# Optimization experiments

Hardware: AMD Instinct MI355X
Metric: run time of the kernel (lower is better)

## Reference

```python
import jax, jax.numpy as jnp
import numpy as np

L = 8       # num_layers
D = 512     # embed_dim
H = 8       # num_heads
HD = D // H # head_dim = 64
V = 256     # vocab_size
T = 2048    # seq len (= context_length)
B = 4       # batch
FF = 4 * D  # mlp hidden
EPS = 1e-5


def setup_inputs() -> dict:
    key = jax.random.key(0)
    ks = jax.random.split(key, 18)
    g = lambda k, shape: (jax.random.normal(k, shape, jnp.float32) * 0.02)
    return {
        "x": jax.random.randint(ks[0], (B, T), 0, V),
        "tok_emb": g(ks[1], (V, D)),
        "pos_emb": g(ks[2], (T, D)),
        "attn_w": g(ks[3], (L, D, 3 * D)),
        "attn_b": g(ks[4], (L, 3 * D)),
        "proj_w": g(ks[5], (L, D, D)),
        "proj_b": g(ks[6], (L, D)),
        "ln1_g": jnp.ones((L, D), jnp.float32),
        "ln1_b": jnp.zeros((L, D), jnp.float32),
        "ln2_g": jnp.ones((L, D), jnp.float32),
        "ln2_b": jnp.zeros((L, D), jnp.float32),
        "ff1_w": g(ks[7], (L, D, FF)),
        "ff1_b": g(ks[8], (L, FF)),
        "ff2_w": g(ks[9], (L, FF, D)),
        "ff2_b": g(ks[10], (L, D)),
        "lnf_g": jnp.ones((D,), jnp.float32),
        "lnf_b": jnp.zeros((D,), jnp.float32),
    }


def _ln(x, g, b):
    m = jnp.mean(x, axis=-1, keepdims=True)
    v = jnp.mean(jnp.square(x - m), axis=-1, keepdims=True)
    return (x - m) * jax.lax.rsqrt(v + EPS) * g + b


def reference(x, tok_emb, pos_emb, attn_w, attn_b, proj_w, proj_b,
              ln1_g, ln1_b, ln2_g, ln2_b, ff1_w, ff1_b, ff2_w, ff2_b,
              lnf_g, lnf_b):
    Bx, Tx = x.shape
    h = tok_emb[x] + pos_emb[:Tx]                     # [B,T,D]
    causal = jnp.tril(jnp.ones((Tx, Tx), bool))       # [T,T]
    scale = 1.0 / np.sqrt(HD)
    for i in range(L):
        hn = _ln(h, ln1_g[i], ln1_b[i])
        qkv = hn @ attn_w[i] + attn_b[i]              # [B,T,3D]
        qkv = qkv.reshape(Bx, Tx, 3, H, HD)
        q = qkv[:, :, 0].transpose(0, 2, 1, 3)        # [B,H,T,HD]
        k = qkv[:, :, 1].transpose(0, 2, 1, 3)
        v = qkv[:, :, 2].transpose(0, 2, 1, 3)
        scores = jnp.einsum('bhqd,bhkd->bhqk', q, k) * scale
        scores = jnp.where(causal, scores, jnp.float32(-1e9))
        attn = jax.nn.softmax(scores, axis=-1)        # dropout identity at eval
        o = jnp.einsum('bhqk,bhkd->bhqd', attn, v)
        o = o.transpose(0, 2, 1, 3).reshape(Bx, Tx, D)
        h = h + o @ proj_w[i] + proj_b[i]
        hn2 = _ln(h, ln2_g[i], ln2_b[i])
        ff = jax.nn.gelu(hn2 @ ff1_w[i] + ff1_b[i], approximate=False)
        h = h + ff @ ff2_w[i] + ff2_b[i]
    logits = _ln(h, lnf_g, lnf_b) @ tok_emb.T         # tied lm_head
    return logits
```

## Files before the change

kernel.cpp:

```cpp
#include <hip/hip_runtime.h>

#define TT 2048
#define BB 4
#define DD 512
#define HH 8
#define LL 8
#define FFD 2048
#define VV 256
#define ROWS (BB*TT)

typedef short bf16x4 __attribute__((ext_vector_type(4)));
typedef short bf16x8 __attribute__((ext_vector_type(8)));
typedef float f32x4 __attribute__((ext_vector_type(4)));

#define GL2LDS(gp, lp) __builtin_amdgcn_global_load_lds( \
    (const __attribute__((address_space(1))) unsigned*)(gp), \
    (__attribute__((address_space(3))) unsigned*)(lp), 16, 0, 0)

__device__ __forceinline__ float bf2f(short s){
  union { unsigned u; float f; } x; x.u = ((unsigned)(unsigned short)s) << 16; return x.f;
}
__device__ __forceinline__ short f2bf(float f){
  union { float f; unsigned u; } x; x.f = f;
  unsigned r = (x.u + 0x7fffu + ((x.u >> 16) & 1u)) >> 16;
  return (short)(unsigned short)r;
}
__device__ __forceinline__ float ex2(float x){
  float r; asm("v_exp_f32 %0, %1" : "=v"(r) : "v"(x)); return r;
}
__device__ __forceinline__ unsigned cvtpk(float lo, float hi){
  unsigned r; asm("v_cvt_pk_bf16_f32 %0, %1, %2" : "=v"(r) : "v"(lo), "v"(hi)); return r;
}
__device__ __forceinline__ float xmax32(float x){ return fmaxf(x, __shfl_xor(x, 32)); }
__device__ __forceinline__ float xadd32(float x){ return x + __shfl_xor(x, 32); }

__global__ __launch_bounds__(128) void embed_kernel(const int* __restrict__ x,
    const float* __restrict__ tok, const float* __restrict__ pos, float* __restrict__ h){
  int row = blockIdx.x;
  int t = row & (TT-1);
  int id = x[row];
  const float4 a = *(const float4*)&tok[(size_t)id*DD + threadIdx.x*4];
  const float4 p = *(const float4*)&pos[(size_t)t*DD + threadIdx.x*4];
  float4 r; r.x=a.x+p.x; r.y=a.y+p.y; r.z=a.z+p.z; r.w=a.w+p.w;
  *(float4*)&h[(size_t)row*DD + threadIdx.x*4] = r;
}

__global__ __launch_bounds__(256) void ln_kernel(const float* __restrict__ xx,
    const float* __restrict__ gw, const float* __restrict__ bw, short* __restrict__ out){
  const int lane = threadIdx.x & 63, w = threadIdx.x >> 6;
  const int row = blockIdx.x*4 + w;
  const float* xp = xx + (size_t)row*DD + lane*8;
  float4 a = *(const float4*)xp, c = *(const float4*)(xp+4);
  float xv[8] = {a.x,a.y,a.z,a.w,c.x,c.y,c.z,c.w};
  float s1 = 0.f, s2 = 0.f;
  #pragma unroll
  for (int e=0;e<8;e++){ s1 += xv[e]; s2 += xv[e]*xv[e]; }
  #pragma unroll
  for (int off=1; off<64; off<<=1){
    s1 += __shfl_xor(s1, off);
    s2 += __shfl_xor(s2, off);
  }
  const float m = s1 * (1.0f/DD);
  const float rstd = rsqrtf(s2*(1.0f/DD) - m*m + 1e-5f);
  const float4 g0 = *(const float4*)(gw + lane*8), g1 = *(const float4*)(gw + lane*8 + 4);
  const float4 b0 = *(const float4*)(bw + lane*8), b1 = *(const float4*)(bw + lane*8 + 4);
  float gg[8] = {g0.x,g0.y,g0.z,g0.w,g1.x,g1.y,g1.z,g1.w};
  float bb[8] = {b0.x,b0.y,b0.z,b0.w,b1.x,b1.y,b1.z,b1.w};
  short r[8];
  #pragma unroll
  for (int e=0;e<8;e++) r[e] = f2bf((xv[e]-m)*rstd*gg[e] + bb[e]);
  *(bf16x8*)&out[(size_t)row*DD + lane*8] = *(const bf16x8*)r;
}

__global__ __launch_bounds__(256) void transpose_cast_kernel(const float* __restrict__ src,
    short* __restrict__ dst, int R, int C){
  __shared__ float tile[32][33];
  size_t off = (size_t)blockIdx.z * R * C;
  src += off; dst += off;
  int c0 = blockIdx.x*32, r0 = blockIdx.y*32;
  int tx = threadIdx.x & 31, ty = threadIdx.x >> 5;
  #pragma unroll
  for (int i=0;i<4;i++) tile[ty + i*8][tx] = src[(size_t)(r0+ty+i*8)*C + c0 + tx];
  __syncthreads();
  #pragma unroll
  for (int i=0;i<4;i++) dst[(size_t)(c0+ty+i*8)*R + r0 + tx] = f2bf(tile[tx][ty+i*8]);
}

__global__ void cast_kernel(const float* __restrict__ in, short* __restrict__ out, int n){
  for (int i = blockIdx.x*blockDim.x + threadIdx.x; i < n; i += gridDim.x*blockDim.x)
    out[i] = f2bf(in[i]);
}

template<int EPI>
__global__ __launch_bounds__(256) void gemm_dma(const short* __restrict__ A,
    const short* __restrict__ BT, const float* __restrict__ bias, void* __restrict__ C,
    int M, int N, int K)
{
  __shared__ short As[128*64];
  __shared__ short Bs[128*64];
  const int gx = gridDim.x, nwg = gx*gridDim.y;
  int lin = blockIdx.y*gx + blockIdx.x;
  lin = (lin & 7)*(nwg >> 3) + (lin >> 3);
  const int row0 = (lin % gx)*128, col0 = (lin / gx)*128;
  const int t = threadIdx.x, lane = t & 63, w = t >> 6;
  const int wm = w >> 1, wn = w & 1;
  const int rr = lane & 15, g = lane >> 4;
  f32x4 acc[4][4];
  #pragma unroll
  for (int m=0;m<4;m++)
    #pragma unroll
    for (int n=0;n<4;n++) acc[m][n] = (f32x4){0.f,0.f,0.f,0.f};

  const short* aP = A  + (size_t)(row0 + w*32 + (lane>>3))*K + (lane&7)*8;
  const short* bP = BT + (size_t)(col0 + w*32 + (lane>>3))*K + (lane&7)*8;
  short* aL = As + w*2048;
  short* bL = Bs + w*2048;

  for (int kt=0; kt<K; kt+=64){
    __syncthreads();
    #pragma unroll
    for (int i=0;i<4;i++){
      GL2LDS(aP + (size_t)i*8*K + kt, aL + i*512);
      GL2LDS(bP + (size_t)i*8*K + kt, bL + i*512);
    }
    __syncthreads();
    #pragma unroll
    for (int ks=0; ks<2; ks++){
      bf16x8 af[4], bfr[4];
      #pragma unroll
      for (int m=0;m<4;m++) af[m]  = *(const bf16x8*)&As[(wm*64 + m*16 + rr)*64 + ks*32 + g*8];
      #pragma unroll
      for (int n=0;n<4;n++) bfr[n] = *(const bf16x8*)&Bs[(wn*64 + n*16 + rr)*64 + ks*32 + g*8];
      #pragma unroll
      for (int m=0;m<4;m++)
        #pragma unroll
        for (int n=0;n<4;n++)
          acc[m][n] = __builtin_amdgcn_mfma_f32_16x16x32_bf16(af[m], bfr[n], acc[m][n], 0,0,0);
    }
  }
  #pragma unroll
  for (int m=0;m<4;m++){
    #pragma unroll
    for (int n=0;n<4;n++){
      int cg = col0 + wn*64 + n*16 + rr;
      float bv = bias[cg];
      #pragma unroll
      for (int i=0;i<4;i++){
        int rg = row0 + wm*64 + m*16 + g*4 + i;
        float v = acc[m][n][i] + bv;
        size_t idx = (size_t)rg*N + cg;
        if constexpr (EPI==1) ((short*)C)[idx] = f2bf(v);
        else if constexpr (EPI==2) { v = 0.5f*v*(1.0f + erff(v*0.70710678118f)); ((short*)C)[idx] = f2bf(v); }
        else { ((float*)C)[idx] += v; }
      }
    }
  }
}

__global__ __launch_bounds__(256) void gemm_dma_n64(const short* __restrict__ A,
    const short* __restrict__ BT, const float* __restrict__ bias, float* __restrict__ C,
    int M, int N, int K)
{
  __shared__ short As[128*64];
  __shared__ short Bs[64*64];
  const int gx = gridDim.x, nwg = gx*gridDim.y;
  int lin = blockIdx.y*gx + blockIdx.x;
  lin = (lin & 7)*(nwg >> 3) + (lin >> 3);
  const int row0 = (lin % gx)*128, col0 = (lin / gx)*64;
  const int t = threadIdx.x, lane = t & 63, w = t >> 6;
  const int wm = w >> 1, wn = w & 1;
  const int rr = lane & 15, g = lane >> 4;
  f32x4 acc[4][2];
  #pragma unroll
  for (int m=0;m<4;m++)
    #pragma unroll
    for (int n=0;n<2;n++) acc[m][n] = (f32x4){0.f,0.f,0.f,0.f};

  const short* aP = A  + (size_t)(row0 + w*32 + (lane>>3))*K + (lane&7)*8;
  const short* bP = BT + (size_t)(col0 + w*16 + (lane>>3))*K + (lane&7)*8;
  short* aL = As + w*2048;
  short* bL = Bs + w*1024;

  for (int kt=0; kt<K; kt+=64){
    __syncthreads();
    #pragma unroll
    for (int i=0;i<4;i++) GL2LDS(aP + (size_t)i*8*K + kt, aL + i*512);
    #pragma unroll
    for (int i=0;i<2;i++) GL2LDS(bP + (size_t)i*8*K + kt, bL + i*512);
    __syncthreads();
    #pragma unroll
    for (int ks=0; ks<2; ks++){
      bf16x8 af[4], bfr[2];
      #pragma unroll
      for (int m=0;m<4;m++) af[m]  = *(const bf16x8*)&As[(wm*64 + m*16 + rr)*64 + ks*32 + g*8];
      #pragma unroll
      for (int n=0;n<2;n++) bfr[n] = *(const bf16x8*)&Bs[(wn*32 + n*16 + rr)*64 + ks*32 + g*8];
      #pragma unroll
      for (int m=0;m<4;m++)
        #pragma unroll
        for (int n=0;n<2;n++)
          acc[m][n] = __builtin_amdgcn_mfma_f32_16x16x32_bf16(af[m], bfr[n], acc[m][n], 0,0,0);
    }
  }
  #pragma unroll
  for (int m=0;m<4;m++){
    #pragma unroll
    for (int n=0;n<2;n++){
      int cg = col0 + wn*32 + n*16 + rr;
      float bv = bias[cg];
      #pragma unroll
      for (int i=0;i<4;i++){
        int rg = row0 + wm*64 + m*16 + g*4 + i;
        C[(size_t)rg*N + cg] += acc[m][n][i] + bv;
      }
    }
  }
}

template<int BM, int BN>
__global__ __launch_bounds__(256) void gemm_small(const short* __restrict__ A,
    const short* __restrict__ BT, float* __restrict__ C, int M, int N, int K)
{
  constexpr int FM = BM/32, FN = BN/32;
  __shared__ short As[BM][72];
  __shared__ short Bs[BN][72];
  const int row0 = blockIdx.x*BM, col0 = blockIdx.y*BN;
  const int t = threadIdx.x, lane = t & 63, w = t >> 6;
  const int wm = w >> 1, wn = w & 1;
  const int rr = lane & 15, kg = (lane >> 4)*8;
  f32x4 acc[FM][FN];
  #pragma unroll
  for (int m=0;m<FM;m++)
    #pragma unroll
    for (int n=0;n<FN;n++) acc[m][n] = (f32x4){0.f,0.f,0.f,0.f};

  for (int kt=0; kt<K; kt+=64){
    #pragma unroll
    for (int i=0;i<BM/32;i++){
      int cid = t + i*256; int r = cid >> 3; int c = (cid & 7)*8;
      *(bf16x8*)&As[r][c] = *(const bf16x8*)&A[(size_t)(row0+r)*K + kt + c];
    }
    #pragma unroll
    for (int i=0;i<BN/32;i++){
      int cid = t + i*256; int r = cid >> 3; int c = (cid & 7)*8;
      *(bf16x8*)&Bs[r][c] = *(const bf16x8*)&BT[(size_t)(col0+r)*K + kt + c];
    }
    __syncthreads();
    #pragma unroll
    for (int ks=0; ks<2; ks++){
      bf16x8 af[FM], bfr[FN];
      #pragma unroll
      for (int m=0;m<FM;m++) af[m] = *(const bf16x8*)&As[wm*FM*16 + m*16 + rr][ks*32 + kg];
      #pragma unroll
      for (int n=0;n<FN;n++) bfr[n] = *(const bf16x8*)&Bs[wn*FN*16 + n*16 + rr][ks*32 + kg];
      #pragma unroll
      for (int m=0;m<FM;m++)
        #pragma unroll
        for (int n=0;n<FN;n++)
          acc[m][n] = __builtin_amdgcn_mfma_f32_16x16x32_bf16(af[m], bfr[n], acc[m][n], 0,0,0);
    }
    __syncthreads();
  }
  #pragma unroll
  for (int m=0;m<FM;m++)
    #pragma unroll
    for (int n=0;n<FN;n++){
      int cg = col0 + wn*FN*16 + n*16 + rr;
      #pragma unroll
      for (int i=0;i<4;i++){
        int rg = row0 + wm*FM*16 + m*16 + (lane>>4)*4 + i;
        C[(size_t)rg*N + cg] = acc[m][n][i];
      }
    }
}

__device__ __forceinline__ void attn_tile(const short* __restrict__ Kc,
    const short* __restrict__ Vc, const bf16x8* qr, f32x4* oacc,
    float& mrun, float& lpart, int qi, int g, int qloc, bool diag)
{
  f32x4 sacc[4];
  #pragma unroll
  for (int f=0; f<4; f++) sacc[f] = (f32x4){0.f,0.f,0.f,0.f};
  __builtin_amdgcn_s_setprio(1);
  #pragma unroll
  for (int ks=0; ks<2; ks++){
    #pragma unroll
    for (int f=0; f<4; f++){
      bf16x8 kf = *(const bf16x8*)&Kc[(f*16 + qi)*64 + (((ks*4 + g) ^ (qi&7))*8)];
      sacc[f] = __builtin_amdgcn_mfma_f32_16x16x32_bf16(kf, qr[ks], sacc[f], 0,0,0);
    }
  }
  __builtin_amdgcn_s_setprio(0);

  float p[4][4];
  if (diag){
    #pragma unroll
    for (int f=0; f<4; f++)
      #pragma unroll
      for (int i=0; i<4; i++){
        int koffs = f*16 + g*4 + i;
        p[f][i] = (koffs <= qloc) ? sacc[f][i] : -1e30f;
      }
  } else {
    #pragma unroll
    for (int f=0; f<4; f++)
      #pragma unroll
      for (int i=0; i<4; i++) p[f][i] = sacc[f][i];
  }
  float t0 = fmaxf(fmaxf(p[0][0],p[0][1]), fmaxf(p[0][2],p[0][3]));
  float t1 = fmaxf(fmaxf(p[1][0],p[1][1]), fmaxf(p[1][2],p[1][3]));
  float t2 = fmaxf(fmaxf(p[2][0],p[2][1]), fmaxf(p[2][2],p[2][3]));
  float t3 = fmaxf(fmaxf(p[3][0],p[3][1]), fmaxf(p[3][2],p[3][3]));
  float tm = fmaxf(fmaxf(t0,t1), fmaxf(t2,t3));
  tm = fmaxf(tm, __shfl_xor(tm, 16));
  tm = xmax32(tm);
  if (!__all(tm <= mrun + 8.f)){
    float mnew = fmaxf(mrun, tm);
    float corr = ex2(mrun - mnew);
    lpart *= corr;
    #pragma unroll
    for (int mf=0; mf<4; mf++)
      #pragma unroll
      for (int i=0; i<4; i++) oacc[mf][i] *= corr;
    mrun = mnew;
  }
  float ts = 0.f;
  #pragma unroll
  for (int f=0; f<4; f++)
    #pragma unroll
    for (int i=0; i<4; i++){
      float e = ex2(p[f][i] - mrun);
      p[f][i] = e;
      ts += e;
    }
  lpart += ts;

  __builtin_amdgcn_s_setprio(1);
  #pragma unroll
  for (int w2=0; w2<2; w2++){
    union { unsigned u[4]; bf16x8 v; } bfr;
    bfr.u[0] = cvtpk(p[2*w2  ][0], p[2*w2  ][1]);
    bfr.u[1] = cvtpk(p[2*w2  ][2], p[2*w2  ][3]);
    bfr.u[2] = cvtpk(p[2*w2+1][0], p[2*w2+1][1]);
    bfr.u[3] = cvtpk(p[2*w2+1][2], p[2*w2+1][3]);
    #pragma unroll
    for (int mf=0; mf<4; mf++){
      const short* vp = &Vc[(mf*16 + qi)*72 + w2*32 + g*4];
      union { bf16x4 h[2]; bf16x8 v; } af;
      af.h[0] = *(const bf16x4*)vp;
      af.h[1] = *(const bf16x4*)(vp + 16);
      oacc[mf] = __builtin_amdgcn_mfma_f32_16x16x32_bf16(af.v, bfr.v, oacc[mf], 0,0,0);
    }
  }
  __builtin_amdgcn_s_setprio(0);
}

__global__ __launch_bounds__(256) void attn_kernel(const short* __restrict__ qkv, short* __restrict__ o){
  __shared__ __align__(16) char smem[34816];
  short* KsB = (short*)smem;
  short* VtB = (short*)(smem + 16384);
  float* Osh = (float*)smem;

  const int lin = blockIdx.x;
  const int xcd = lin & 7, idx = lin >> 3;
  const int bh = xcd*4 + (idx & 3);
  const int qp = idx >> 2;
  const int b = bh >> 3, hh = bh & 7;
  const int ql = qp, qh = 31 - qp;
  const int nt = qh + 1;

  const int t = threadIdx.x, lane = t & 63, wid = t >> 6;
  const int g = lane >> 4, qi = lane & 15;
  const int qloc = wid*16 + qi;
  const size_t base = (size_t)b*TT*3*DD + hh*64;

  bf16x8 qL[2], qH[2];
  {
    const float qs = 0.125f * 1.44269504f;
    const short* qpL = qkv + base + (size_t)(ql*64 + qloc)*3*DD + g*8;
    const short* qpH = qkv + base + (size_t)(qh*64 + qloc)*3*DD + g*8;
    qL[0] = *(const bf16x8*)&qpL[0]; qL[1] = *(const bf16x8*)&qpL[32];
    qH[0] = *(const bf16x8*)&qpH[0]; qH[1] = *(const bf16x8*)&qpH[32];
    #pragma unroll
    for (int j=0;j<8;j++){
      qL[0][j] = f2bf(qs * bf2f(qL[0][j]));
      qL[1][j] = f2bf(qs * bf2f(qL[1][j]));
      qH[0][j] = f2bf(qs * bf2f(qH[0][j]));
      qH[1][j] = f2bf(qs * bf2f(qH[1][j]));
    }
  }
  f32x4 oL[4], oH[4];
  #pragma unroll
  for (int mf=0; mf<4; mf++){ oL[mf] = (f32x4){0.f,0.f,0.f,0.f}; oH[mf] = (f32x4){0.f,0.f,0.f,0.f}; }
  float mL = -1e30f, lL = 0.f, mH = -1e30f, lH = 0.f;

  const short* ksrc = qkv + base + DD + (size_t)(wid*16 + (lane>>3))*3*DD
                      + (((lane&7) ^ (lane>>3))*8);
  const int vk = (t & 31)*2, vd = (t >> 5)*8;
  const short* vsrc = qkv + base + 2*DD + (size_t)vk*3*DD + vd;

  GL2LDS(ksrc, KsB + wid*1024);
  GL2LDS(ksrc + (size_t)8*3*DD, KsB + wid*1024 + 512);
  bf16x8 v0a = *(const bf16x8*)vsrc;
  bf16x8 v0b = *(const bf16x8*)(vsrc + 3*DD);
  bf16x8 vLoA = *(const bf16x8*)(vsrc + (size_t)64*3*DD);
  bf16x8 vLoB = *(const bf16x8*)(vsrc + (size_t)64*3*DD + 3*DD);
  asm volatile("s_waitcnt vmcnt(0)" ::: "memory");
  #pragma unroll
  for (int e=0;e<8;e++)
    *(unsigned*)&VtB[(vd+e)*72 + vk] =
        (unsigned)(unsigned short)v0a[e] | ((unsigned)(unsigned short)v0b[e] << 16);

  for (int kb = 0; kb < nt; kb++){
    asm volatile("s_waitcnt vmcnt(0) lgkmcnt(0)\n\ts_barrier" ::: "memory");
    bf16x8 vHiA = vLoA, vHiB = vLoB;
    if (kb+1 < nt){
      const size_t koff = (size_t)(kb+1)*64*3*DD;
      short* kd = KsB + ((kb+1)&1)*4096 + wid*1024;
      GL2LDS(ksrc + koff, kd);
      GL2LDS(ksrc + koff + (size_t)8*3*DD, kd + 512);
      short* Vn = VtB + ((kb+1)&1)*4608;
      #pragma unroll
      for (int e=0;e<8;e++)
        *(unsigned*)&Vn[(vd+e)*72 + vk] =
            (unsigned)(unsigned short)vLoA[e] | ((unsigned)(unsigned short)vLoB[e] << 16);
    }
    if (kb+2 < nt){
      const size_t koff2 = (size_t)(kb+2)*64*3*DD;
      vHiA = *(const bf16x8*)(vsrc + koff2);
      vHiB = *(const bf16x8*)(vsrc + koff2 + 3*DD);
    }
    const short* Kc = KsB + (kb&1)*4096;
    const short* Vc = VtB + (kb&1)*4608;

    attn_tile(Kc, Vc, qH, oH, mH, lH, qi, g, qloc, kb == nt-1);
    if (kb <= ql)
      attn_tile(Kc, Vc, qL, oL, mL, lL, qi, g, qloc, kb == ql);

    vLoA = vHiA; vLoB = vHiB;
  }

  lL += __shfl_xor(lL, 16); lL = xadd32(lL);
  lH += __shfl_xor(lH, 16); lH = xadd32(lH);

  const int orow = t >> 2, cc = (t & 3) * 16;
  #pragma unroll
  for (int s=0; s<2; s++){
    const f32x4* oacc = s ? oH : oL;
    const float inv = 1.f / (s ? lH : lL);
    const int q0 = (s ? qh : ql) * 64;
    __syncthreads();
    #pragma unroll
    for (int mf=0; mf<4; mf++)
      #pragma unroll
      for (int i=0; i<4; i++)
        Osh[qloc*65 + mf*16 + g*4 + i] = oacc[mf][i] * inv;
    __syncthreads();
    short tmp[16];
    #pragma unroll
    for (int e=0; e<16; e++) tmp[e] = f2bf(Osh[orow*65 + cc + e]);
    short* op = o + ((size_t)b*TT + q0 + orow)*DD + hh*64 + cc;
    *(bf16x8*)&op[0] = *(const bf16x8*)&tmp[0];
    *(bf16x8*)&op[8] = *(const bf16x8*)&tmp[8];
  }
}

extern "C" void kernel_launch(void* const* d_in, const int* in_sizes, int n_in,
                              void* d_out, int out_size, void* d_ws, size_t ws_size,
                              hipStream_t stream) {
  const int*   x      = (const int*)d_in[0];
  const float* tok    = (const float*)d_in[1];
  const float* pos    = (const float*)d_in[2];
  const float* attn_w = (const float*)d_in[3];
  const float* attn_b = (const float*)d_in[4];
  const float* proj_w = (const float*)d_in[5];
  const float* proj_b = (const float*)d_in[6];
  const float* ln1_g  = (const float*)d_in[7];
  const float* ln1_b  = (const float*)d_in[8];
  const float* ln2_g  = (const float*)d_in[9];
  const float* ln2_b  = (const float*)d_in[10];
  const float* ff1_w  = (const float*)d_in[11];
  const float* ff1_b  = (const float*)d_in[12];
  const float* ff2_w  = (const float*)d_in[13];
  const float* ff2_b  = (const float*)d_in[14];
  const float* lnf_g  = (const float*)d_in[15];
  const float* lnf_b  = (const float*)d_in[16];

  char* p = (char*)d_ws;
  float* h   = (float*)p; p += (size_t)ROWS*DD*4;
  short* hn  = (short*)p; p += (size_t)ROWS*DD*2;
  short* qkv = (short*)p; p += (size_t)ROWS*3*DD*2;
  short* ob  = (short*)p; p += (size_t)ROWS*DD*2;
  short* ffb = (short*)p; p += (size_t)ROWS*FFD*2;
  short* awT = (short*)p; p += (size_t)LL*3*DD*DD*2;
  short* pwT = (short*)p; p += (size_t)LL*DD*DD*2;
  short* f1T = (short*)p; p += (size_t)LL*FFD*DD*2;
  short* f2T = (short*)p; p += (size_t)LL*DD*FFD*2;
  short* lmT = (short*)p; p += (size_t)VV*DD*2;

  transpose_cast_kernel<<<dim3(48,16,8),256,0,stream>>>(attn_w, awT, DD, 3*DD);
  transpose_cast_kernel<<<dim3(16,16,8),256,0,stream>>>(proj_w, pwT, DD, DD);
  transpose_cast_kernel<<<dim3(64,16,8),256,0,stream>>>(ff1_w, f1T, DD, FFD);
  transpose_cast_kernel<<<dim3(16,64,8),256,0,stream>>>(ff2_w, f2T, FFD, DD);
  cast_kernel<<<128,256,0,stream>>>(tok, lmT, VV*DD);
  embed_kernel<<<ROWS,128,0,stream>>>(x, tok, pos, h);

  for (int l=0;l<LL;l++){
    ln_kernel<<<ROWS/4,256,0,stream>>>(h, ln1_g + l*DD, ln1_b + l*DD, hn);
    gemm_dma<1><<<dim3(ROWS/128, (3*DD)/128),256,0,stream>>>(
        hn, awT + (size_t)l*3*DD*DD, attn_b + (size_t)l*3*DD, qkv, ROWS, 3*DD, DD);
    attn_kernel<<<512,256,0,stream>>>(qkv, ob);
    gemm_dma_n64<<<dim3(ROWS/128, DD/64),256,0,stream>>>(
        ob, pwT + (size_t)l*DD*DD, proj_b + (size_t)l*DD, h, ROWS, DD, DD);
    ln_kernel<<<ROWS/4,256,0,stream>>>(h, ln2_g + l*DD, ln2_b + l*DD, hn);
    gemm_dma<2><<<dim3(ROWS/128, FFD/128),256,0,stream>>>(
        hn, f1T + (size_t)l*FFD*DD, ff1_b + (size_t)l*FFD, ffb, ROWS, FFD, DD);
    gemm_dma_n64<<<dim3(ROWS/128, DD/64),256,0,stream>>>(
        ffb, f2T + (size_t)l*DD*FFD, ff2_b + (size_t)l*DD, h, ROWS, DD, FFD);
  }
  ln_kernel<<<ROWS/4,256,0,stream>>>(h, lnf_g, lnf_b, hn);
  gemm_small<64,64><<<dim3(ROWS/64, VV/64),256,0,stream>>>(
      hn, lmT, (float*)d_out, ROWS, VV, DD);
}
```

Measured before the change: 1.643 ms.

## Double-buffer LDS tiles in bf16 GEMM and remap tiles to per-XCD row bands

The main GEMM now keeps two LDS buffers, so the global-to-LDS DMA for the next K tile is issued before the MFMA work on the current tile. This replaces the two barriers per iteration with one explicit waitcnt+barrier and is meant to hide load latency. Both GEMMs also get a new block-to-tile mapping that gives each XCD a contiguous band of rows and walks columns inside it, aiming for better L2 reuse of the A rows. The cost is twice the LDS (64KB per block), which may lower occupancy.

```diff
diff --git a/kernel.cpp b/kernel.cpp
--- a/kernel.cpp
+++ b/kernel.cpp
@@ -91,17 +91,24 @@
     out[i] = f2bf(in[i]);
 }
 
+__device__ __forceinline__ void xcd_rowband(int gx, int gy, int& rowt, int& colt){
+  int lin = blockIdx.y*gx + blockIdx.x;
+  int x = lin & 7, j = lin >> 3;
+  int jd = j / gy;
+  rowt = x*(gx >> 3) + jd;
+  colt = j - jd*gy;
+}
+
 template<int EPI>
 __global__ __launch_bounds__(256) void gemm_dma(const short* __restrict__ A,
     const short* __restrict__ BT, const float* __restrict__ bias, void* __restrict__ C,
     int M, int N, int K)
 {
-  __shared__ short As[128*64];
-  __shared__ short Bs[128*64];
-  const int gx = gridDim.x, nwg = gx*gridDim.y;
-  int lin = blockIdx.y*gx + blockIdx.x;
-  lin = (lin & 7)*(nwg >> 3) + (lin >> 3);
-  const int row0 = (lin % gx)*128, col0 = (lin / gx)*128;
+  __shared__ short As[2][128*64];
+  __shared__ short Bs[2][128*64];
+  int rowt, colt;
+  xcd_rowband(gridDim.x, gridDim.y, rowt, colt);
+  const int row0 = rowt*128, col0 = colt*128;
   const int t = threadIdx.x, lane = t & 63, w = t >> 6;
   const int wm = w >> 1, wn = w & 1;
   const int rr = lane & 15, g = lane >> 4;
@@ -113,24 +120,32 @@
 
   const short* aP = A  + (size_t)(row0 + w*32 + (lane>>3))*K + (lane&7)*8;
   const short* bP = BT + (size_t)(col0 + w*32 + (lane>>3))*K + (lane&7)*8;
-  short* aL = As + w*2048;
-  short* bL = Bs + w*2048;
-
-  for (int kt=0; kt<K; kt+=64){
-    __syncthreads();
-    #pragma unroll
-    for (int i=0;i<4;i++){
-      GL2LDS(aP + (size_t)i*8*K + kt, aL + i*512);
-      GL2LDS(bP + (size_t)i*8*K + kt, bL + i*512);
-    }
-    __syncthreads();
+
+  const int nk = K >> 6;
+  #pragma unroll
+  for (int i=0;i<4;i++){
+    GL2LDS(aP + (size_t)i*8*K, &As[0][w*2048 + i*512]);
+    GL2LDS(bP + (size_t)i*8*K, &Bs[0][w*2048 + i*512]);
+  }
+  for (int kt=0; kt<nk; kt++){
+    asm volatile("s_waitcnt vmcnt(0) lgkmcnt(0)\n\ts_barrier" ::: "memory");
+    if (kt+1 < nk){
+      const int ko = (kt+1) << 6, nb = (kt+1) & 1;
+      #pragma unroll
+      for (int i=0;i<4;i++){
+        GL2LDS(aP + (size_t)i*8*K + ko, &As[nb][w*2048 + i*512]);
+        GL2LDS(bP + (size_t)i*8*K + ko, &Bs[nb][w*2048 + i*512]);
+      }
+    }
+    const short* Ac = As[kt&1];
+    const short* Bc = Bs[kt&1];
     #pragma unroll
     for (int ks=0; ks<2; ks++){
       bf16x8 af[4], bfr[4];
       #pragma unroll
-      for (int m=0;m<4;m++) af[m]  = *(const bf16x8*)&As[(wm*64 + m*16 + rr)*64 + ks*32 + g*8];
-      #pragma unroll
-      for (int n=0;n<4;n++) bfr[n] = *(const bf16x8*)&Bs[(wn*64 + n*16 + rr)*64 + ks*32 + g*8];
+      for (int m=0;m<4;m++) af[m]  = *(const bf16x8*)&Ac[(wm*64 + m*16 + rr)*64 + ks*32 + g*8];
+      #pragma unroll
+      for (int n=0;n<4;n++) bfr[n] = *(const bf16x8*)&Bc[(wn*64 + n*16 + rr)*64 + ks*32 + g*8];
       #pragma unroll
       for (int m=0;m<4;m++)
         #pragma unroll
@@ -163,10 +178,9 @@
 {
   __shared__ short As[128*64];
   __shared__ short Bs[64*64];
-  const int gx = gridDim.x, nwg = gx*gridDim.y;
-  int lin = blockIdx.y*gx + blockIdx.x;
-  lin = (lin & 7)*(nwg >> 3) + (lin >> 3);
-  const int row0 = (lin % gx)*128, col0 = (lin / gx)*64;
+  int rowt, colt;
+  xcd_rowband(gridDim.x, gridDim.y, rowt, colt);
+  const int row0 = rowt*128, col0 = colt*64;
   const int t = threadIdx.x, lane = t & 63, w = t >> 6;
   const int wm = w >> 1, wn = w & 1;
   const int rr = lane & 15, g = lane >> 4;
```

Result: faster. 1.572 ms (-4.3%).
